# Kernel tuning notes

Hardware: AMD Instinct MI355X
Metric: run time of the kernel (lower is better)

## Reference

```python
import jax, jax.numpy as jnp
import numpy as np

B, N, QD = 2, 2048, 1024
HEADS, DIM_HEAD = 16, 64
INNER = HEADS * DIM_HEAD  # 1024
SCALE = DIM_HEAD ** -0.5


def setup_inputs() -> dict:
    key = jax.random.key(0)
    ks = jax.random.split(key, 8)
    x = jax.random.normal(ks[0], (B, N, QD), dtype=jnp.float32)
    bias = jax.random.normal(ks[1], (B, N, N), dtype=jnp.float32)
    mask = jax.random.randint(ks[2], (B, N), 0, 2) > 0
    # parameters (nn.Linear stores weight [out, in]; we keep [in, out] and matmul x @ W)
    Wq = jax.random.normal(ks[3], (QD, INNER), dtype=jnp.float32) * (QD ** -0.5)
    Wkv = jax.random.normal(ks[4], (QD, 2 * INNER), dtype=jnp.float32) * (QD ** -0.5)
    Wo = jax.random.normal(ks[5], (INNER, QD), dtype=jnp.float32) * (INNER ** -0.5)
    bo = jax.random.normal(ks[6], (QD,), dtype=jnp.float32) * 0.01
    return {"x": x, "bias": bias, "mask": mask, "Wq": Wq, "Wkv": Wkv, "Wo": Wo, "bo": bo}


def reference(x, bias, mask, Wq, Wkv, Wo, bo):
    b, n, _ = x.shape
    q = x @ Wq                      # [b, n, inner]
    kv = x @ Wkv                    # [b, n, 2*inner] (context defaults to x)
    k, v = jnp.split(kv, 2, axis=-1)
    # split heads: [b, h, n, d]
    split = lambda t: t.reshape(b, n, HEADS, DIM_HEAD).transpose(0, 2, 1, 3)
    q, k, v = split(q), split(k), split(v)
    sim = jnp.einsum('bhid,bhjd->bhij', q, k) * SCALE   # [b, h, n, n]
    sim = sim + bias[:, None, :, :]                      # additive bias broadcast over heads
    max_neg = -jnp.finfo(sim.dtype).max
    sim = jnp.where(mask[:, None, None, :], sim, max_neg)  # per-key mask
    attn = jax.nn.softmax(sim, axis=-1)
    out = jnp.einsum('bhij,bhjd->bhid', attn, v)         # [b, h, n, d]
    out = out.transpose(0, 2, 1, 3).reshape(b, n, INNER)  # merge heads
    return out @ Wo + bo
```

## Files before the change

### kernel.cpp

```cpp
#include <hip/hip_runtime.h>
#include <hip/hip_bf16.h>
#include <stdint.h>

#define B_     2
#define N_     2048
#define QD_    1024
#define H_     16
#define DH_    64
#define INNER_ 1024
#define SCALE_ 0.125f

typedef unsigned short u16;
typedef __attribute__((ext_vector_type(8))) short bf16x8;
typedef __attribute__((ext_vector_type(4))) float f32x4;
typedef __attribute__((ext_vector_type(4))) unsigned short u16x4;
typedef __attribute__((ext_vector_type(8))) unsigned short u16x8;

#define GLD16(gp, lp) __builtin_amdgcn_global_load_lds( \
    (const __attribute__((address_space(1))) unsigned int*)(gp), \
    (__attribute__((address_space(3))) unsigned int*)(lp), 16, 0, 0)

__device__ inline u16 f2bf(float f) {
    union { float f; uint32_t u; } c; c.f = f;
    uint32_t r = c.u + 0x7FFFu + ((c.u >> 16) & 1u);
    return (u16)(r >> 16);
}
__device__ inline float bf2f(u16 s) {
    union { uint32_t u; float f; } c; c.u = ((uint32_t)s) << 16;
    return c.f;
}
__device__ inline void split2(float v, u16 &h, u16 &l) {
    u16 hs = f2bf(v);
    h = hs;
    l = f2bf(v - bf2f(hs));
}
__device__ inline unsigned pk2(float a, float b) {
    float2 f; f.x = a; f.y = b;
    union { __hip_bfloat162 v; unsigned u; } c;
    c.v = __float22bfloat162_rn(f);
    return c.u;
}
__device__ inline float f4get(const float4& v, int r) {
    return r == 0 ? v.x : r == 1 ? v.y : r == 2 ? v.z : v.w;
}

__global__ __launch_bounds__(256) void prep_kernel(
    const float* __restrict__ x, u16* __restrict__ xh, u16* __restrict__ xl,
    const float* __restrict__ Wq, const float* __restrict__ Wkv, const float* __restrict__ Wo,
    u16* __restrict__ wTh, u16* __restrict__ wTl,
    u16* __restrict__ woTh, u16* __restrict__ woTl)
{
    __shared__ float t[32][33];
    const int blk = blockIdx.x, tid = threadIdx.x;
    if (blk < 4096) {
        int idx = blk * 256 + tid;
        float4 v = ((const float4*)x)[idx];
        u16x4 hv, lv; u16 h, l;
        split2(v.x, h, l); hv.x = h; lv.x = l;
        split2(v.y, h, l); hv.y = h; lv.y = l;
        split2(v.z, h, l); hv.z = h; lv.z = l;
        split2(v.w, h, l); hv.w = h; lv.w = l;
        ((u16x4*)xh)[idx] = hv;
        ((u16x4*)xl)[idx] = lv;
        return;
    }
    int local = blk - 4096;
    const float* src; u16 *dhi, *dlo; int C, bx, by;
    if (local < 1024)      { src = Wq;  dhi = wTh;                dlo = wTl;                C = 1024; by = local >> 5; bx = local & 31; }
    else if (local < 3072) { int l2 = local - 1024; src = Wkv; dhi = wTh + 1024 * 1024; dlo = wTl + 1024 * 1024; C = 2048; by = l2 >> 6; bx = l2 & 63; }
    else                   { int l2 = local - 3072; src = Wo;  dhi = woTh;               dlo = woTl;               C = 1024; by = l2 >> 5; bx = l2 & 31; }
    const int x0 = bx * 32, y0 = by * 32;
    const int tx = tid & 31, ty = tid >> 5;
    for (int yy = ty; yy < 32; yy += 8)
        t[yy][tx] = src[(size_t)(y0 + yy) * C + x0 + tx];
    __syncthreads();
    for (int i = ty; i < 32; i += 8) {
        float v = t[tx][i];
        u16 h, l; split2(v, h, l);
        size_t o = (size_t)(x0 + i) * 1024 + y0 + tx;
        dhi[o] = h; dlo[o] = l;
    }
}

__device__ inline void bias_read(int T, int bkoff, int bl16,
                                 const float* __restrict__ bias,
                                 const int* __restrict__ mask,
                                 float4 bR[4], int4& bM)
{
    int bb2 = T >> 10, rest = T & 1023;
    int k0b = (rest & 31) * 64, q0 = (rest >> 5) * 64;
    int kk = k0b + bkoff;
    bM = *(const int4*)&mask[bb2 * N_ + kk];
#pragma unroll
    for (int m = 0; m < 4; m++)
        bR[m] = *(const float4*)&bias[((size_t)bb2 * N_ + q0 + m * 16 + bl16) * N_ + kk];
}
__device__ inline void bias_store(int T, int bwvr, int blane, int bhf,
                                  const float4 bR[4], const int4& bM,
                                  u16* __restrict__ bsw)
{
    int bb2 = T >> 10, rest = T & 1023;
    int k0b = (rest & 31) * 64, q0 = (rest >> 5) * 64;
    int wv = ((k0b >> 5) & 3) + bwvr;
    const u16 NEG = f2bf(-1e30f);
    const int mok[4] = { bM.x, bM.y, bM.z, bM.w };
    u16x8 o0, o1;
#pragma unroll
    for (int i = 0; i < 8; i++) {
        int m = i >> 2, r = i & 3;
        o0[i] = mok[r] ? f2bf(f4get(bR[m], r)) : NEG;
    }
#pragma unroll
    for (int i = 0; i < 8; i++) {
        int m = 2 + (i >> 2), r = i & 3;
        o1[i] = mok[r] ? f2bf(f4get(bR[m], r)) : NEG;
    }
    size_t ob = ((((size_t)bb2 * 32 + (q0 >> 6)) * 16 + (k0b >> 7)) * 4 + wv) * 2048
                + (size_t)blane * 32 + bhf * 16;
    *(u16x8*)&bsw[ob]     = o0;
    *(u16x8*)&bsw[ob + 8] = o1;
}

__global__ __launch_bounds__(256) void gemm_qkv_bias(
    int mode,
    const u16* __restrict__ Ah, const u16* __restrict__ Al,
    const u16* __restrict__ Bh,
    u16* __restrict__ qh,
    u16* __restrict__ kb, u16* __restrict__ vT,
    const float* __restrict__ bias, const int* __restrict__ mask,
    u16* __restrict__ bsw)
{
    __shared__ __align__(16) char smem[49152];
    const int tid = threadIdx.x;

    if (mode == 2) {
        const int bid = blockIdx.x;
        const int bp = tid >> 1, bhf = tid & 1;
        const int blane = bp & 63, bquad = blane >> 4, bl16 = blane & 15;
        const int bwvr = bp >> 6;
        const int bkoff = bwvr * 32 + bquad * 8 + bhf * 4;
        float4 bR[4]; int4 bM;
        bias_read(bid, bkoff, bl16, bias, mask, bR, bM);
        bias_store(bid, bwvr, blane, bhf, bR, bM, bsw);
        return;
    }
    const int gid = blockIdx.x;

    const int wave = tid >> 6, lane = tid & 63;
    const int quad = lane >> 4, l16 = lane & 15;
    const int wm = wave >> 1, wn = wave & 1;
    const int bx = gid % 24, by = gid / 24;
    const int bm = by * 128, bn = bx * 128;
    const bool comp = (bx < 8);

    f32x4 acc[4][4];
#pragma unroll
    for (int i = 0; i < 4; i++)
#pragma unroll
        for (int j = 0; j < 4; j++) acc[i][j] = (f32x4){0.f, 0.f, 0.f, 0.f};

    const int row0 = tid >> 2, g4 = tid & 3;
    const int r1 = row0, r2 = row0 + 64;
    const int gc1 = (g4 ^ (r1 & 3)) * 8, gc2 = (g4 ^ (r2 & 3)) * 8;
    const size_t a1 = (size_t)(bm + r1) * 1024 + gc1, a2 = (size_t)(bm + r2) * 1024 + gc2;
    const size_t b1 = (size_t)(bn + r1) * 1024 + gc1, b2 = (size_t)(bn + r2) * 1024 + gc2;
    const int ldsw = wave * 1024;

    auto issue = [&](char* base, int kn) {
        GLD16(Ah + a1 + kn, base + ldsw);
        GLD16(Ah + a2 + kn, base + 4096 + ldsw);
        GLD16(Bh + b1 + kn, base + 16384 + ldsw);
        GLD16(Bh + b2 + kn, base + 20480 + ldsw);
        if (comp) {
            GLD16(Al + a1 + kn, base + 8192 + ldsw);
            GLD16(Al + a2 + kn, base + 12288 + ldsw);
        }
    };

    const int bp = tid >> 1, bhf = tid & 1;
    const int blane = bp & 63, bquad = blane >> 4, bl16 = blane & 15;
    const int bwvr = bp >> 6;
    const int bkoff = bwvr * 32 + bquad * 8 + bhf * 4;
    float4 bR[4]; int4 bM;

    issue(smem, 0);
    int cur = 0;
    for (int k0 = 0; k0 < 1024; k0 += 32) {
        __syncthreads();
        char* cb_ = smem + cur * 24576;
        if (k0 + 32 < 1024) issue(smem + (cur ^ 1) * 24576, k0 + 32);
        if (mode == 1) {
            const int kstep = k0 >> 5;
            if (kstep == 1)  bias_read (gid,        bkoff, bl16, bias, mask, bR, bM);
            if (kstep == 9)  bias_store(gid,        bwvr, blane, bhf, bR, bM, bsw);
            if (kstep == 11) bias_read (gid + 768,  bkoff, bl16, bias, mask, bR, bM);
            if (kstep == 19) bias_store(gid + 768,  bwvr, blane, bhf, bR, bM, bsw);
            if (kstep == 21 && gid < 512) bias_read (gid + 1536, bkoff, bl16, bias, mask, bR, bM);
            if (kstep == 29 && gid < 512) bias_store(gid + 1536, bwvr, blane, bhf, bR, bM, bsw);
        }
        const u16* cAh = (const u16*)cb_;
        const u16* cAl = (const u16*)(cb_ + 8192);
        const u16* cBh = (const u16*)(cb_ + 16384);
        bf16x8 fah[4], fal[4], fbh[4];
#pragma unroll
        for (int s = 0; s < 4; s++) {
            int ra = wm * 64 + s * 16 + l16;
            int rb = wn * 64 + s * 16 + l16;
            int ca = (quad ^ (ra & 3)) * 8;
            int cb = (quad ^ (rb & 3)) * 8;
            fah[s] = *(const bf16x8*)&cAh[ra * 32 + ca];
            fbh[s] = *(const bf16x8*)&cBh[rb * 32 + cb];
            if (comp) fal[s] = *(const bf16x8*)&cAl[ra * 32 + ca];
        }
#pragma unroll
        for (int sm = 0; sm < 4; sm++)
#pragma unroll
            for (int sn = 0; sn < 4; sn++) {
                acc[sm][sn] = __builtin_amdgcn_mfma_f32_16x16x32_bf16(fah[sm], fbh[sn], acc[sm][sn], 0, 0, 0);
                if (comp)
                    acc[sm][sn] = __builtin_amdgcn_mfma_f32_16x16x32_bf16(fal[sm], fbh[sn], acc[sm][sn], 0, 0, 0);
            }
        cur ^= 1;
    }
#pragma unroll
    for (int sm = 0; sm < 4; sm++) {
        int rowb = bm + wm * 64 + sm * 16 + quad * 4;
        int bb = rowb >> 11, i0 = rowb & 2047;
#pragma unroll
        for (int sn = 0; sn < 4; sn++) {
            int col = bn + wn * 64 + sn * 16 + l16;
            int region = col >> 10;
            int hh = (col >> 6) & 15;
            int d = col & 63;
            if (region == 0) {
#pragma unroll
                for (int r = 0; r < 4; r++) {
                    size_t o = (((size_t)(bb * H_ + hh)) * N_ + i0 + r) * DH_ + d;
                    qh[o] = f2bf(acc[sm][sn][r] * SCALE_);
                }
            } else if (region == 1) {
#pragma unroll
                for (int r = 0; r < 4; r++) {
                    size_t o = (((size_t)(bb * H_ + hh)) * N_ + i0 + r) * DH_ + d;
                    kb[o] = f2bf(acc[sm][sn][r]);
                }
            } else {
                u16x4 pv;
#pragma unroll
                for (int r = 0; r < 4; r++) pv[r] = f2bf(acc[sm][sn][r]);
                *(u16x4*)&vT[(((size_t)(bb * H_ + hh)) * DH_ + d) * N_ + i0] = pv;
            }
        }
    }
}

__global__ __launch_bounds__(256) void gemm_out(
    const u16* __restrict__ Ab,
    const u16* __restrict__ Bh,
    const float* __restrict__ bo, float* __restrict__ out)
{
    __shared__ __align__(16) char smem[24576];
    const int tid = threadIdx.x;
    const int wave = tid >> 6, lane = tid & 63;
    const int quad = lane >> 4, l16 = lane & 15;
    const int wm = wave >> 1, wn = wave & 1;
    const int bm = blockIdx.y * 128, bn = blockIdx.x * 64;

    f32x4 acc[4][2];
#pragma unroll
    for (int i = 0; i < 4; i++)
#pragma unroll
        for (int j = 0; j < 2; j++) acc[i][j] = (f32x4){0.f, 0.f, 0.f, 0.f};

    const int row0 = tid >> 2, g4 = tid & 3;
    const int r1 = row0, r2 = row0 + 64;
    const int gc1 = (g4 ^ (r1 & 3)) * 8, gc2 = (g4 ^ (r2 & 3)) * 8;
    const size_t a1 = (size_t)(bm + r1) * 1024 + gc1, a2 = (size_t)(bm + r2) * 1024 + gc2;
    const size_t bgo = (size_t)(bn + r1) * 1024 + gc1;
    const int ldsw = wave * 1024;

    auto issue = [&](char* base, int kn) {
        GLD16(Ab + a1 + kn, base + ldsw);
        GLD16(Ab + a2 + kn, base + 4096 + ldsw);
        GLD16(Bh + bgo + kn, base + 8192 + ldsw);
    };

    issue(smem, 0);
    int cur = 0;
    for (int k0 = 0; k0 < 1024; k0 += 32) {
        __syncthreads();
        char* cb_ = smem + cur * 12288;
        if (k0 + 32 < 1024) issue(smem + (cur ^ 1) * 12288, k0 + 32);
        const u16* cA  = (const u16*)cb_;
        const u16* cBh = (const u16*)(cb_ + 8192);
        bf16x8 fa[4], fbh[2];
#pragma unroll
        for (int s = 0; s < 4; s++) {
            int ra = wm * 64 + s * 16 + l16;
            int ca = (quad ^ (ra & 3)) * 8;
            fa[s] = *(const bf16x8*)&cA[ra * 32 + ca];
        }
#pragma unroll
        for (int s = 0; s < 2; s++) {
            int rb = wn * 32 + s * 16 + l16;
            int cb = (quad ^ (rb & 3)) * 8;
            fbh[s] = *(const bf16x8*)&cBh[rb * 32 + cb];
        }
#pragma unroll
        for (int sm = 0; sm < 4; sm++)
#pragma unroll
            for (int sn = 0; sn < 2; sn++)
                acc[sm][sn] = __builtin_amdgcn_mfma_f32_16x16x32_bf16(fa[sm], fbh[sn], acc[sm][sn], 0, 0, 0);
        cur ^= 1;
    }
#pragma unroll
    for (int sm = 0; sm < 4; sm++) {
        int rowb = bm + wm * 64 + sm * 16 + quad * 4;
#pragma unroll
        for (int sn = 0; sn < 2; sn++) {
            int col = bn + wn * 32 + sn * 16 + l16;
            float bv = bo[col];
#pragma unroll
            for (int r = 0; r < 4; r++)
                out[(size_t)(rowb + r) * 1024 + col] = acc[sm][sn][r] + bv;
        }
    }
}

#define LDK 72
#define LDV 128

__global__ __launch_bounds__(256, 2) void attn_kernel(
    const u16* __restrict__ qh,
    const u16* __restrict__ kb, const u16* __restrict__ vT,
    const u16* __restrict__ bsw, u16* __restrict__ ob)
{
    __shared__ __align__(16) char smem[35328];
    u16* sK  = (u16*)smem;
    u16* sVt = (u16*)(smem + 18432);
    float* rO = (float*)smem;
    float* rL = (float*)(smem + 34816);

    const int bh = blockIdx.y, b = bh >> 4, h = bh & 15;
    const int qt = blockIdx.x, qbase = qt * 64;
    const int tid = threadIdx.x, wave = tid >> 6, lane = tid & 63;
    const int quad = lane >> 4, l16 = lane & 15;

    bf16x8 aq[4][2];
#pragma unroll
    for (int m = 0; m < 4; m++) {
        size_t qo = ((size_t)bh * N_ + qbase + m * 16 + l16) * DH_ + quad * 8;
        aq[m][0] = *(const bf16x8*)&qh[qo];
        aq[m][1] = *(const bf16x8*)&qh[qo + 32];
    }
    f32x4 Oacc[4][4], lacc[4];
#pragma unroll
    for (int m = 0; m < 4; m++) {
        lacc[m] = (f32x4){0.f, 0.f, 0.f, 0.f};
#pragma unroll
        for (int nd = 0; nd < 4; nd++) Oacc[m][nd] = (f32x4){0.f, 0.f, 0.f, 0.f};
    }
    bf16x8 ones;
#pragma unroll
    for (int i = 0; i < 8; i++) ones[i] = (short)0x3F80;

    const int rK = tid >> 3, cK = (tid & 7) * 8;
    const int sigK = ((rK & 4) << 2) + ((rK >> 3) << 2) + (rK & 3);
    const int rV = tid >> 4;
    const int vg = tid & 15;
    const int cV = vg * 8;
    const int vsw = (vg ^ (rV & 7)) * 8;
    const int vrg = ((wave * 4 + quad) ^ (l16 & 7)) * 8;
    const size_t kgbase = (size_t)bh * N_ * DH_;
    const size_t vgbase = (size_t)bh * DH_ * N_;
    const size_t bswb = (size_t)(b * 32 + qt) * 131072 + (size_t)wave * 2048
                        + (size_t)lane * 32;

    bf16x8 pK[4], pV[4];
    u16x8 cB[4], nB[4];
#pragma unroll
    for (int it = 0; it < 4; it++) {
        pK[it] = *(const bf16x8*)&kb[kgbase + (size_t)(rK + it * 32) * DH_ + cK];
        pV[it] = *(const bf16x8*)&vT[vgbase + (size_t)(rV + it * 16) * N_ + cV];
    }
#pragma unroll
    for (int c = 0; c < 4; c++) cB[c] = *(const u16x8*)&bsw[bswb + c * 8];

    for (int jt = 0; jt < 16; jt++) {
#pragma unroll
        for (int it = 0; it < 4; it++) {
            *(bf16x8*)&sK[(it * 32 + sigK) * LDK + cK] = pK[it];
            *(bf16x8*)&sVt[(rV + it * 16) * LDV + vsw] = pV[it];
        }
        __syncthreads();
        {
            int jn = (jt + 1) & 15;
            int j0n = jn * 128;
#pragma unroll
            for (int it = 0; it < 4; it++) {
                pK[it] = *(const bf16x8*)&kb[kgbase + (size_t)(j0n + rK + it * 32) * DH_ + cK];
                pV[it] = *(const bf16x8*)&vT[vgbase + (size_t)(rV + it * 16) * N_ + j0n + cV];
            }
            size_t bb = bswb + (size_t)jn * 8192;
#pragma unroll
            for (int c = 0; c < 4; c++) nB[c] = *(const u16x8*)&bsw[bb + c * 8];
        }
        bf16x8 kf[2][2], vf[4];
#pragma unroll
        for (int n = 0; n < 2; n++)
#pragma unroll
            for (int s = 0; s < 2; s++)
                kf[n][s] = *(const bf16x8*)&sK[(wave * 32 + n * 16 + l16) * LDK + s * 32 + quad * 8];
#pragma unroll
        for (int nd = 0; nd < 4; nd++)
            vf[nd] = *(const bf16x8*)&sVt[(nd * 16 + l16) * LDV + vrg];

#pragma unroll
        for (int m = 0; m < 4; m++) {
            f32x4 S0 = (f32x4){0.f, 0.f, 0.f, 0.f};
            f32x4 S1 = (f32x4){0.f, 0.f, 0.f, 0.f};
#pragma unroll
            for (int s = 0; s < 2; s++) {
                S0 = __builtin_amdgcn_mfma_f32_16x16x32_bf16(kf[0][s], aq[m][s], S0, 0, 0, 0);
                S1 = __builtin_amdgcn_mfma_f32_16x16x32_bf16(kf[1][s], aq[m][s], S1, 0, 0, 0);
            }
            float p0[4], p1[4];
#pragma unroll
            for (int r = 0; r < 4; r++) {
                p0[r] = __expf(S0[r] + bf2f(cB[m >> 1][(m & 1) * 4 + r]));
                p1[r] = __expf(S1[r] + bf2f(cB[2 + (m >> 1)][(m & 1) * 4 + r]));
            }
            union { bf16x8 v; unsigned w[4]; } pa;
            pa.w[0] = pk2(p0[0], p0[1]);
            pa.w[1] = pk2(p0[2], p0[3]);
            pa.w[2] = pk2(p1[0], p1[1]);
            pa.w[3] = pk2(p1[2], p1[3]);
            lacc[m] = __builtin_amdgcn_mfma_f32_16x16x32_bf16(pa.v, ones, lacc[m], 0, 0, 0);
#pragma unroll
            for (int nd = 0; nd < 4; nd++)
                Oacc[m][nd] = __builtin_amdgcn_mfma_f32_16x16x32_bf16(pa.v, vf[nd], Oacc[m][nd], 0, 0, 0);
        }
#pragma unroll
        for (int c = 0; c < 4; c++) cB[c] = nB[c];
        __syncthreads();
    }

    if (wave >= 2) {
        int slot = wave - 2;
#pragma unroll
        for (int m = 0; m < 4; m++) {
#pragma unroll
            for (int nd = 0; nd < 4; nd++)
#pragma unroll
                for (int r = 0; r < 4; r++)
                    rO[(slot * 64 + m * 16 + quad * 4 + r) * 68 + nd * 16 + l16] = Oacc[m][nd][r];
            if (l16 == 0)
#pragma unroll
                for (int r = 0; r < 4; r++)
                    rL[slot * 64 + m * 16 + quad * 4 + r] = lacc[m][r];
        }
    }
    __syncthreads();
    if (wave < 2) {
        int slot = wave;
#pragma unroll
        for (int m = 0; m < 4; m++) {
#pragma unroll
            for (int nd = 0; nd < 4; nd++)
#pragma unroll
                for (int r = 0; r < 4; r++) {
                    int idx = (slot * 64 + m * 16 + quad * 4 + r) * 68 + nd * 16 + l16;
                    rO[idx] += Oacc[m][nd][r];
                }
            if (l16 == 0)
#pragma unroll
                for (int r = 0; r < 4; r++)
                    rL[slot * 64 + m * 16 + quad * 4 + r] += lacc[m][r];
        }
    }
    __syncthreads();
    {
        const int q = tid >> 2, dg = (tid & 3) * 16;
        float l = rL[q] + rL[64 + q];
        float inv = 1.f / l;
        f32x4 s[4];
#pragma unroll
        for (int i4 = 0; i4 < 4; i4++) {
            s[i4] = *(const f32x4*)&rO[(size_t)q * 68 + dg + i4 * 4];
            f32x4 v = *(const f32x4*)&rO[(size_t)(64 + q) * 68 + dg + i4 * 4];
            s[i4] += v;
        }
        size_t obase = ((size_t)b * N_ + qbase + q) * INNER_ + h * 64 + dg;
#pragma unroll
        for (int i4 = 0; i4 < 4; i4++) {
            u16x4 o4;
#pragma unroll
            for (int r = 0; r < 4; r++) o4[r] = f2bf(s[i4][r] * inv);
            *(u16x4*)&ob[obase + i4 * 4] = o4;
        }
    }
}

extern "C" void kernel_launch(void* const* d_in, const int* in_sizes, int n_in,
                              void* d_out, int out_size, void* d_ws, size_t ws_size,
                              hipStream_t stream)
{
    const float* x    = (const float*)d_in[0];
    const float* bias = (const float*)d_in[1];
    const int*   mask = (const int*)d_in[2];
    const float* Wq   = (const float*)d_in[3];
    const float* Wkv  = (const float*)d_in[4];
    const float* Wo   = (const float*)d_in[5];
    const float* bo   = (const float*)d_in[6];
    float* out = (float*)d_out;

    char* w = (char*)d_ws;
    const size_t MB = 1024 * 1024;
    u16* q_h   = (u16*)(w);
    u16* k_b   = (u16*)(w + 16 * MB);
    u16* v_T   = (u16*)(w + 24 * MB);
    u16* xs_h  = (u16*)(w + 32 * MB);
    u16* xs_l  = (u16*)(w + 40 * MB);
    u16* wT_h  = (u16*)(w + 48 * MB);
    u16* wT_l  = (u16*)(w + 54 * MB);
    u16* woT_h = (u16*)(w + 60 * MB);
    u16* woT_l = (u16*)(w + 62 * MB);
    u16* o_b   = (u16*)(w + 64 * MB);

    const size_t bsw_bytes = (size_t)2 * N_ * N_ * sizeof(u16);
    const bool concurrent = ws_size >= 72 * MB + bsw_bytes;

    prep_kernel<<<8192, 256, 0, stream>>>(x, xs_h, xs_l, Wq, Wkv, Wo, wT_h, wT_l, woT_h, woT_l);

    if (concurrent) {
        u16* bsw = (u16*)(w + 72 * MB);
        gemm_qkv_bias<<<768, 256, 0, stream>>>(1, xs_h, xs_l, wT_h,
                                               q_h, k_b, v_T, bias, mask, bsw);
        attn_kernel<<<dim3(32, 32), 256, 0, stream>>>(q_h, k_b, v_T, bsw, o_b);
    } else {
        u16* bsw = (u16*)(w + 32 * MB);
        gemm_qkv_bias<<<768, 256, 0, stream>>>(0, xs_h, xs_l, wT_h,
                                               q_h, k_b, v_T, bias, mask, bsw);
        gemm_qkv_bias<<<2048, 256, 0, stream>>>(2, xs_h, xs_l, wT_h,
                                                q_h, k_b, v_T, bias, mask, bsw);
        attn_kernel<<<dim3(32, 32), 256, 0, stream>>>(q_h, k_b, v_T, bsw, o_b);
    }
    gemm_out<<<dim3(16, 32), 256, 0, stream>>>(o_b, woT_h, bo, out);
}
```

Before: 266.3 us.

## Split bias preprocessing into its own kernel and raise attention occupancy bound

Removes the bias/mask conversion that was interleaved into the QKV GEMM main loop, so the GEMM runs without the extra loads and stores and their register pressure. A separate bias kernel now always runs between the GEMM and attention. The attention kernel's launch bound is raised from 2 to 4 blocks per CU, which pushes the compiler toward fewer registers per thread and risks spills. The separate kernel gives up the overlap of bias traffic with GEMM compute and adds one launch.

```diff
diff --git a/kernel.cpp b/kernel.cpp
--- a/kernel.cpp
+++ b/kernel.cpp
@@ -121,29 +121,28 @@
     *(u16x8*)&bsw[ob + 8] = o1;
 }
 
-__global__ __launch_bounds__(256) void gemm_qkv_bias(
-    int mode,
+__global__ __launch_bounds__(256) void bias_kernel(
+    const float* __restrict__ bias, const int* __restrict__ mask,
+    u16* __restrict__ bsw)
+{
+    const int bid = blockIdx.x, tid = threadIdx.x;
+    const int bp = tid >> 1, bhf = tid & 1;
+    const int blane = bp & 63, bquad = blane >> 4, bl16 = blane & 15;
+    const int bwvr = bp >> 6;
+    const int bkoff = bwvr * 32 + bquad * 8 + bhf * 4;
+    float4 bR[4]; int4 bM;
+    bias_read(bid, bkoff, bl16, bias, mask, bR, bM);
+    bias_store(bid, bwvr, blane, bhf, bR, bM, bsw);
+}
+
+__global__ __launch_bounds__(256) void gemm_qkv(
     const u16* __restrict__ Ah, const u16* __restrict__ Al,
     const u16* __restrict__ Bh,
     u16* __restrict__ qh,
-    u16* __restrict__ kb, u16* __restrict__ vT,
-    const float* __restrict__ bias, const int* __restrict__ mask,
-    u16* __restrict__ bsw)
+    u16* __restrict__ kb, u16* __restrict__ vT)
 {
     __shared__ __align__(16) char smem[49152];
     const int tid = threadIdx.x;
-
-    if (mode == 2) {
-        const int bid = blockIdx.x;
-        const int bp = tid >> 1, bhf = tid & 1;
-        const int blane = bp & 63, bquad = blane >> 4, bl16 = blane & 15;
-        const int bwvr = bp >> 6;
-        const int bkoff = bwvr * 32 + bquad * 8 + bhf * 4;
-        float4 bR[4]; int4 bM;
-        bias_read(bid, bkoff, bl16, bias, mask, bR, bM);
-        bias_store(bid, bwvr, blane, bhf, bR, bM, bsw);
-        return;
-    }
     const int gid = blockIdx.x;
 
     const int wave = tid >> 6, lane = tid & 63;
@@ -177,27 +176,12 @@
         }
     };
 
-    const int bp = tid >> 1, bhf = tid & 1;
-    const int blane = bp & 63, bquad = blane >> 4, bl16 = blane & 15;
-    const int bwvr = bp >> 6;
-    const int bkoff = bwvr * 32 + bquad * 8 + bhf * 4;
-    float4 bR[4]; int4 bM;
-
     issue(smem, 0);
     int cur = 0;
     for (int k0 = 0; k0 < 1024; k0 += 32) {
         __syncthreads();
         char* cb_ = smem + cur * 24576;
         if (k0 + 32 < 1024) issue(smem + (cur ^ 1) * 24576, k0 + 32);
-        if (mode == 1) {
-            const int kstep = k0 >> 5;
-            if (kstep == 1)  bias_read (gid,        bkoff, bl16, bias, mask, bR, bM);
-            if (kstep == 9)  bias_store(gid,        bwvr, blane, bhf, bR, bM, bsw);
-            if (kstep == 11) bias_read (gid + 768,  bkoff, bl16, bias, mask, bR, bM);
-            if (kstep == 19) bias_store(gid + 768,  bwvr, blane, bhf, bR, bM, bsw);
-            if (kstep == 21 && gid < 512) bias_read (gid + 1536, bkoff, bl16, bias, mask, bR, bM);
-            if (kstep == 29 && gid < 512) bias_store(gid + 1536, bwvr, blane, bhf, bR, bM, bsw);
-        }
         const u16* cAh = (const u16*)cb_;
         const u16* cAl = (const u16*)(cb_ + 8192);
         const u16* cBh = (const u16*)(cb_ + 16384);
@@ -330,7 +314,7 @@
 #define LDK 72
 #define LDV 128
 
-__global__ __launch_bounds__(256, 2) void attn_kernel(
+__global__ __launch_bounds__(256, 4) void attn_kernel(
     const u16* __restrict__ qh,
     const u16* __restrict__ kb, const u16* __restrict__ vT,
     const u16* __restrict__ bsw, u16* __restrict__ ob)
@@ -530,20 +514,11 @@
     const size_t bsw_bytes = (size_t)2 * N_ * N_ * sizeof(u16);
     const bool concurrent = ws_size >= 72 * MB + bsw_bytes;
 
+    u16* bsw = concurrent ? (u16*)(w + 72 * MB) : (u16*)(w + 32 * MB);
+
     prep_kernel<<<8192, 256, 0, stream>>>(x, xs_h, xs_l, Wq, Wkv, Wo, wT_h, wT_l, woT_h, woT_l);
-
-    if (concurrent) {
-        u16* bsw = (u16*)(w + 72 * MB);
-        gemm_qkv_bias<<<768, 256, 0, stream>>>(1, xs_h, xs_l, wT_h,
-                                               q_h, k_b, v_T, bias, mask, bsw);
-        attn_kernel<<<dim3(32, 32), 256, 0, stream>>>(q_h, k_b, v_T, bsw, o_b);
-    } else {
-        u16* bsw = (u16*)(w + 32 * MB);
-        gemm_qkv_bias<<<768, 256, 0, stream>>>(0, xs_h, xs_l, wT_h,
-                                               q_h, k_b, v_T, bias, mask, bsw);
-        gemm_qkv_bias<<<2048, 256, 0, stream>>>(2, xs_h, xs_l, wT_h,
-                                                q_h, k_b, v_T, bias, mask, bsw);
-        attn_kernel<<<dim3(32, 32), 256, 0, stream>>>(q_h, k_b, v_T, bsw, o_b);
-    }
+    gemm_qkv<<<768, 256, 0, stream>>>(xs_h, xs_l, wT_h, q_h, k_b, v_T);
+    bias_kernel<<<2048, 256, 0, stream>>>(bias, mask, bsw);
+    attn_kernel<<<dim3(32, 32), 256, 0, stream>>>(q_h, k_b, v_T, bsw, o_b);
     gemm_out<<<dim3(16, 32), 256, 0, stream>>>(o_b, woT_h, bo, out);
 }
```

Result: slower. 523.9 us (+96.8%).
